# Optimization experiments

Measured on AMD Instinct MI355X. Metric: run time of the kernel, lower is better.

## Reference

```python
import jax, jax.numpy as jnp
import numpy as np

B, N, K, F, OUT = 32, 2000, 32, 64, 128

def setup_inputs() -> dict:
    key = jax.random.key(0)
    k1, k2, k3, k4, k5 = jax.random.split(key, 5)
    x = jax.random.normal(k1, (B, N, F), dtype=jnp.float32)
    neighborhood = jax.random.randint(k2, (N, K), 0, N, dtype=jnp.int64)
    distances = jax.random.uniform(k3, (N, K), dtype=jnp.float32)
    # Linear(k*(F+1), OUT): torch default init scale ~ 1/sqrt(fan_in)
    fan_in = K * (F + 1)
    W = jax.random.normal(k4, (OUT, fan_in), dtype=jnp.float32) / np.sqrt(fan_in)
    b = jax.random.normal(k5, (OUT,), dtype=jnp.float32) / np.sqrt(fan_in)
    return {"x": x, "neighborhood": neighborhood, "distances": distances, "W": W, "b": b}

def reference(x, neighborhood, distances, W, b):
    batch, seq_len, feat = x.shape          # [B, N, F]
    k = neighborhood.shape[1]
    gathered = x[:, neighborhood, :]        # [B, N, K, F] gather over sequence dim
    d = jnp.broadcast_to(distances[None, :, :, None], (batch, seq_len, k, 1))
    h = jnp.concatenate([gathered, d], axis=-1)        # [B, N, K, F+1]
    h = h.reshape(batch, seq_len, k * (feat + 1))      # [B, N, K*(F+1)]
    out = jnp.einsum('bnf,of->bno', h, W) + b          # [B, N, OUT]
    return out
```

## Files before the change

kernel.cpp:

```cpp
#include <hip/hip_runtime.h>
#include <hip/hip_bf16.h>
#include <stdint.h>

typedef __attribute__((ext_vector_type(8)))  __bf16   bf16x8;
typedef __attribute__((ext_vector_type(16))) float    f32x16;
typedef __attribute__((ext_vector_type(4)))  float    f32x4;

#define NB   32
#define NN   2000
#define NK   32
#define NF   64
#define NOUT 128
#define NSTEP 130

#define GLOBAL_AS __attribute__((address_space(1)))
#define LDS_AS    __attribute__((address_space(3)))

__global__ void kprep_x(const float* __restrict__ x, const float* __restrict__ dist,
                        __bf16* __restrict__ xb2, __bf16* __restrict__ db) {
  const int n = blockIdx.x;
  const int t = threadIdx.x;
  const int bb = t >> 3;
  const int f0 = (t & 7) << 3;
  const float* src = x + ((size_t)bb * NN + n) * NF + f0;
  f32x4 v0 = *(const f32x4*)(src);
  f32x4 v1 = *(const f32x4*)(src + 4);
  bf16x8 r;
  r[0] = (__bf16)v0[0]; r[1] = (__bf16)v0[1]; r[2] = (__bf16)v0[2]; r[3] = (__bf16)v0[3];
  r[4] = (__bf16)v1[0]; r[5] = (__bf16)v1[1]; r[6] = (__bf16)v1[2]; r[7] = (__bf16)v1[3];
  const int off = ((f0 >> 4) << 10) + (((f0 >> 3) & 1) << 9) + (bb << 4);
  *(bf16x8*)((char*)xb2 + ((size_t)n << 12) + off) = r;
  if (t < NK) db[n * NK + t] = (__bf16)dist[n * NK + t];
}

__global__ void kprep_w(const float* __restrict__ W, __bf16* __restrict__ Wf) {
  const int kstep = blockIdx.x;
  const int t = threadIdx.x;
  const int lane = t & 63;
  const int wv = t >> 6;
  const int o = wv * 32 + (lane & 31);
  const int kbase = kstep * 16 + (lane >> 5) * 8;
  bf16x8 r;
#pragma unroll
  for (int j = 0; j < 8; ++j) {
    const int kg = kbase + j;
    const int col = (kg < 2048) ? ((kg >> 6) * 65 + (kg & 63)) : ((kg - 2048) * 65 + 64);
    r[j] = (__bf16)W[(size_t)o * 2080 + col];
  }
  *(bf16x8*)(Wf + (((size_t)kstep * 256 + t) << 3)) = r;
}

__global__ __launch_bounds__(256, 4) void kmain(
    const int* __restrict__ nbrs, const float* __restrict__ bias,
    const __bf16* __restrict__ xb2, const __bf16* __restrict__ Wf,
    const __bf16* __restrict__ db, float* __restrict__ out) {
  __shared__ __align__(16) char lds[2][16384];

  const int n0   = blockIdx.x * 2;
  const int t    = threadIdx.x;
  const int lane = t & 63;
  const int w    = t >> 6;
  const int col  = lane & 31;
  const int half = lane >> 5;
  const int g    = w >> 1;
  const int c    = w & 1;

  f32x16 acc0 = {};
  f32x16 acc1 = {};

  int myidx = 0;
  if (lane < 16) myidx = nbrs[(n0 + g) * NK + lane * 2 + c];

  const __bf16* wfp = Wf + (((size_t)(w * 64 + lane)) << 3);

  auto stage = [&](int buf, int chunk) {
    const int nb = __builtin_amdgcn_readlane(myidx, chunk);
    const char* gsrc = (const char*)xb2 + ((size_t)nb << 12) + lane * 16;
    char* ldst = &lds[buf][w << 12];
#pragma unroll
    for (int q = 0; q < 4; ++q) {
      __builtin_amdgcn_global_load_lds(
          (const GLOBAL_AS uint32_t*)(gsrc + (q << 10)),
          (LDS_AS uint32_t*)(ldst + (q << 10)), 16, 0, 0);
    }
  };

  auto compute = [&](int buf, int chunk) {
#pragma unroll
    for (int cc = 0; cc < 2; ++cc) {
#pragma unroll
      for (int s = 0; s < 4; ++s) {
        const int kstep = (chunk * 2 + cc) * 4 + s;
        bf16x8 bfr = *(const bf16x8*)(wfp + ((size_t)kstep << 11));
        bf16x8 a0 = *(const bf16x8*)&lds[buf][((0 * 2 + cc) << 12) + (s << 10) + lane * 16];
        bf16x8 a1 = *(const bf16x8*)&lds[buf][((1 * 2 + cc) << 12) + (s << 10) + lane * 16];
        acc0 = __builtin_amdgcn_mfma_f32_32x32x16_bf16(a0, bfr, acc0, 0, 0, 0);
        acc1 = __builtin_amdgcn_mfma_f32_32x32x16_bf16(a1, bfr, acc1, 0, 0, 0);
      }
    }
  };

  stage(0, 0);
  int cur = 0;
  for (int chunk = 0; chunk < 15; ++chunk) {
    stage(cur ^ 1, chunk + 1);
    asm volatile("s_waitcnt vmcnt(4)" ::: "memory");
    __builtin_amdgcn_s_barrier();
    compute(cur, chunk);
    asm volatile("s_waitcnt lgkmcnt(0)" ::: "memory");
    __builtin_amdgcn_s_barrier();
    cur ^= 1;
  }
  asm volatile("s_waitcnt vmcnt(0)" ::: "memory");
  __builtin_amdgcn_s_barrier();
  compute(cur, 15);

#pragma unroll
  for (int s = 0; s < 2; ++s) {
    bf16x8 bfr = *(const bf16x8*)(wfp + ((size_t)(128 + s) << 11));
    bf16x8 dv0 = *(const bf16x8*)((const char*)db + (size_t)n0 * 64 + s * 32 + half * 16);
    bf16x8 dv1 = *(const bf16x8*)((const char*)db + ((size_t)n0 + 1) * 64 + s * 32 + half * 16);
    acc0 = __builtin_amdgcn_mfma_f32_32x32x16_bf16(dv0, bfr, acc0, 0, 0, 0);
    acc1 = __builtin_amdgcn_mfma_f32_32x32x16_bf16(dv1, bfr, acc1, 0, 0, 0);
  }

  const int o = w * 32 + col;
  const float bv = bias[o];
#pragma unroll
  for (int r = 0; r < 16; ++r) {
    const int row = (r & 3) + 8 * (r >> 2) + 4 * half;
    out[((size_t)row * NN + n0) * NOUT + o]     = acc0[r] + bv;
    out[((size_t)row * NN + n0 + 1) * NOUT + o] = acc1[r] + bv;
  }
}

extern "C" void kernel_launch(void* const* d_in, const int* in_sizes, int n_in,
                              void* d_out, int out_size, void* d_ws, size_t ws_size,
                              hipStream_t stream) {
  const float* x    = (const float*)d_in[0];
  const int*   nbrs = (const int*)d_in[1];
  const float* dist = (const float*)d_in[2];
  const float* W    = (const float*)d_in[3];
  const float* bias = (const float*)d_in[4];
  float* out = (float*)d_out;

  char* ws = (char*)d_ws;
  __bf16* xb2 = (__bf16*)(ws);
  __bf16* Wf  = (__bf16*)(ws + 8192000);
  __bf16* db  = (__bf16*)(ws + 8192000 + 532480);

  kprep_x<<<NN, 256, 0, stream>>>(x, dist, xb2, db);
  kprep_w<<<NSTEP, 256, 0, stream>>>(W, Wf);
  kmain<<<NN / 2, 256, 0, stream>>>(nbrs, bias, xb2, Wf, db, out);
}
```

Measured before the change: 62.81 us.

## Process four nodes per block with 4-stage LDS pipeline and fused prep kernel

The main kernel now computes four output nodes per block instead of two, so each W fragment loaded from global memory feeds four MFMAs instead of two. The gather of neighbor rows moves to a 4-buffer LDS ring with three chunks in flight, and W fragments are double-buffered in registers. The x and W preprocessing kernels are merged into one launch, and the x layout is changed to a simpler contiguous per-thread store. In exchange, the block count is halved and launch bounds drop to 2 blocks per CU, which reduces parallelism and occupancy.

```diff
diff --git a/kernel.cpp b/kernel.cpp
--- a/kernel.cpp
+++ b/kernel.cpp
@@ -4,7 +4,7 @@
 
 typedef __attribute__((ext_vector_type(8)))  __bf16   bf16x8;
 typedef __attribute__((ext_vector_type(16))) float    f32x16;
-typedef __attribute__((ext_vector_type(4)))  float    f32x4;
+typedef __attribute__((ext_vector_type(8)))  float    f32x8;
 
 #define NB   32
 #define NN   2000
@@ -16,112 +16,143 @@
 #define GLOBAL_AS __attribute__((address_space(1)))
 #define LDS_AS    __attribute__((address_space(3)))
 
-__global__ void kprep_x(const float* __restrict__ x, const float* __restrict__ dist,
-                        __bf16* __restrict__ xb2, __bf16* __restrict__ db) {
-  const int n = blockIdx.x;
+__global__ void kprep(const float* __restrict__ x, const float* __restrict__ dist,
+                      const float* __restrict__ W,
+                      __bf16* __restrict__ xb2, __bf16* __restrict__ db,
+                      __bf16* __restrict__ Wf) {
   const int t = threadIdx.x;
-  const int bb = t >> 3;
-  const int f0 = (t & 7) << 3;
-  const float* src = x + ((size_t)bb * NN + n) * NF + f0;
-  f32x4 v0 = *(const f32x4*)(src);
-  f32x4 v1 = *(const f32x4*)(src + 4);
-  bf16x8 r;
-  r[0] = (__bf16)v0[0]; r[1] = (__bf16)v0[1]; r[2] = (__bf16)v0[2]; r[3] = (__bf16)v0[3];
-  r[4] = (__bf16)v1[0]; r[5] = (__bf16)v1[1]; r[6] = (__bf16)v1[2]; r[7] = (__bf16)v1[3];
-  const int off = ((f0 >> 4) << 10) + (((f0 >> 3) & 1) << 9) + (bb << 4);
-  *(bf16x8*)((char*)xb2 + ((size_t)n << 12) + off) = r;
-  if (t < NK) db[n * NK + t] = (__bf16)dist[n * NK + t];
+  if (blockIdx.x < NN) {
+    const int n = blockIdx.x;
+    const int col = t & 31, half = (t >> 5) & 1, s = t >> 6;
+    const float* src = x + ((size_t)col * NN + n) * NF + s * 16 + half * 8;
+    f32x8 v = *(const f32x8*)src;
+    bf16x8 r;
+#pragma unroll
+    for (int j = 0; j < 8; ++j) r[j] = (__bf16)v[j];
+    *(bf16x8*)((char*)xb2 + ((size_t)n << 12) + t * 16) = r;
+    if (t < NK) db[n * NK + t] = (__bf16)dist[n * NK + t];
+  } else {
+    const int kstep = blockIdx.x - NN;
+    const int lane = t & 63;
+    const int wv = t >> 6;
+    const int o = wv * 32 + (lane & 31);
+    const int kbase = kstep * 16 + (lane >> 5) * 8;
+    bf16x8 r;
+#pragma unroll
+    for (int j = 0; j < 8; ++j) {
+      const int kg = kbase + j;
+      const int c = (kg < 2048) ? ((kg >> 6) * 65 + (kg & 63)) : ((kg - 2048) * 65 + 64);
+      r[j] = (__bf16)W[(size_t)o * 2080 + c];
+    }
+    *(bf16x8*)(Wf + (((size_t)kstep * 256 + t) << 3)) = r;
+  }
 }
 
-__global__ void kprep_w(const float* __restrict__ W, __bf16* __restrict__ Wf) {
-  const int kstep = blockIdx.x;
-  const int t = threadIdx.x;
-  const int lane = t & 63;
-  const int wv = t >> 6;
-  const int o = wv * 32 + (lane & 31);
-  const int kbase = kstep * 16 + (lane >> 5) * 8;
-  bf16x8 r;
-#pragma unroll
-  for (int j = 0; j < 8; ++j) {
-    const int kg = kbase + j;
-    const int col = (kg < 2048) ? ((kg >> 6) * 65 + (kg & 63)) : ((kg - 2048) * 65 + 64);
-    r[j] = (__bf16)W[(size_t)o * 2080 + col];
-  }
-  *(bf16x8*)(Wf + (((size_t)kstep * 256 + t) << 3)) = r;
-}
-
-__global__ __launch_bounds__(256, 4) void kmain(
+__global__ __launch_bounds__(256, 2) void kmain(
     const int* __restrict__ nbrs, const float* __restrict__ bias,
     const __bf16* __restrict__ xb2, const __bf16* __restrict__ Wf,
     const __bf16* __restrict__ db, float* __restrict__ out) {
-  __shared__ __align__(16) char lds[2][16384];
+  __shared__ __align__(16) char lds[4][4][4096];
 
-  const int n0   = blockIdx.x * 2;
+  const int n0   = blockIdx.x * 4;
   const int t    = threadIdx.x;
   const int lane = t & 63;
   const int w    = t >> 6;
   const int col  = lane & 31;
   const int half = lane >> 5;
-  const int g    = w >> 1;
-  const int c    = w & 1;
 
-  f32x16 acc0 = {};
-  f32x16 acc1 = {};
+  f32x16 acc0 = {}, acc1 = {}, acc2 = {}, acc3 = {};
 
   int myidx = 0;
-  if (lane < 16) myidx = nbrs[(n0 + g) * NK + lane * 2 + c];
+  if (lane < NK) myidx = nbrs[(n0 + w) * NK + lane];
 
   const __bf16* wfp = Wf + (((size_t)(w * 64 + lane)) << 3);
 
-  auto stage = [&](int buf, int chunk) {
-    const int nb = __builtin_amdgcn_readlane(myidx, chunk);
-    const char* gsrc = (const char*)xb2 + ((size_t)nb << 12) + lane * 16;
-    char* ldst = &lds[buf][w << 12];
+  auto stage = [&](int buf, int c) {
+    const int nb = __builtin_amdgcn_readlane(myidx, c);
+    const char* g = (const char*)xb2 + ((size_t)nb << 12) + lane * 16;
+    char* l = &lds[buf][w][0];
 #pragma unroll
-    for (int q = 0; q < 4; ++q) {
+    for (int q = 0; q < 4; ++q)
       __builtin_amdgcn_global_load_lds(
-          (const GLOBAL_AS uint32_t*)(gsrc + (q << 10)),
-          (LDS_AS uint32_t*)(ldst + (q << 10)), 16, 0, 0);
+          (const GLOBAL_AS uint32_t*)(g + (q << 10)),
+          (LDS_AS uint32_t*)(l + (q << 10)), 16, 0, 0);
+  };
+
+  auto loadB = [&](bf16x8* B, int i) {
+#pragma unroll
+    for (int s = 0; s < 4; ++s)
+      B[s] = *(const bf16x8*)(wfp + ((size_t)(i * 4 + s) << 11));
+  };
+
+  auto compute = [&](int buf, const bf16x8* B) {
+#pragma unroll
+    for (int s = 0; s < 4; ++s) {
+      const char* lb = &lds[buf][0][0] + (s << 10) + lane * 16;
+      bf16x8 a0 = *(const bf16x8*)(lb);
+      bf16x8 a1 = *(const bf16x8*)(lb + 4096);
+      bf16x8 a2 = *(const bf16x8*)(lb + 8192);
+      bf16x8 a3 = *(const bf16x8*)(lb + 12288);
+      acc0 = __builtin_amdgcn_mfma_f32_32x32x16_bf16(a0, B[s], acc0, 0, 0, 0);
+      acc1 = __builtin_amdgcn_mfma_f32_32x32x16_bf16(a1, B[s], acc1, 0, 0, 0);
+      acc2 = __builtin_amdgcn_mfma_f32_32x32x16_bf16(a2, B[s], acc2, 0, 0, 0);
+      acc3 = __builtin_amdgcn_mfma_f32_32x32x16_bf16(a3, B[s], acc3, 0, 0, 0);
     }
   };
 
-  auto compute = [&](int buf, int chunk) {
-#pragma unroll
-    for (int cc = 0; cc < 2; ++cc) {
-#pragma unroll
-      for (int s = 0; s < 4; ++s) {
-        const int kstep = (chunk * 2 + cc) * 4 + s;
-        bf16x8 bfr = *(const bf16x8*)(wfp + ((size_t)kstep << 11));
-        bf16x8 a0 = *(const bf16x8*)&lds[buf][((0 * 2 + cc) << 12) + (s << 10) + lane * 16];
-        bf16x8 a1 = *(const bf16x8*)&lds[buf][((1 * 2 + cc) << 12) + (s << 10) + lane * 16];
-        acc0 = __builtin_amdgcn_mfma_f32_32x32x16_bf16(a0, bfr, acc0, 0, 0, 0);
-        acc1 = __builtin_amdgcn_mfma_f32_32x32x16_bf16(a1, bfr, acc1, 0, 0, 0);
-      }
-    }
-  };
+  bf16x8 BA[4], BB[4];
 
-  stage(0, 0);
-  int cur = 0;
-  for (int chunk = 0; chunk < 15; ++chunk) {
-    stage(cur ^ 1, chunk + 1);
-    asm volatile("s_waitcnt vmcnt(4)" ::: "memory");
+  stage(0, 0); stage(1, 1); stage(2, 2);
+  loadB(BA, 0);
+
+  for (int i = 0; i < 28; i += 2) {
     __builtin_amdgcn_s_barrier();
-    compute(cur, chunk);
-    asm volatile("s_waitcnt lgkmcnt(0)" ::: "memory");
+    stage((i + 3) & 3, i + 3);
+    loadB(BB, i + 1);
+    asm volatile("s_waitcnt vmcnt(8)" ::: "memory");
     __builtin_amdgcn_s_barrier();
-    cur ^= 1;
+    compute(i & 3, BA);
+
+    __builtin_amdgcn_s_barrier();
+    stage((i + 4) & 3, i + 4);
+    loadB(BA, i + 2);
+    asm volatile("s_waitcnt vmcnt(8)" ::: "memory");
+    __builtin_amdgcn_s_barrier();
+    compute((i + 1) & 3, BB);
   }
+  __builtin_amdgcn_s_barrier();
+  stage(31 & 3, 31);
+  loadB(BB, 29);
+  asm volatile("s_waitcnt vmcnt(8)" ::: "memory");
+  __builtin_amdgcn_s_barrier();
+  compute(28 & 3, BA);
+  __builtin_amdgcn_s_barrier();
+  loadB(BA, 30);
+  asm volatile("s_waitcnt vmcnt(8)" ::: "memory");
+  __builtin_amdgcn_s_barrier();
+  compute(29 & 3, BB);
+  __builtin_amdgcn_s_barrier();
+  loadB(BB, 31);
+  asm volatile("s_waitcnt vmcnt(4)" ::: "memory");
+  __builtin_amdgcn_s_barrier();
+  compute(30 & 3, BA);
+  __builtin_amdgcn_s_barrier();
   asm volatile("s_waitcnt vmcnt(0)" ::: "memory");
   __builtin_amdgcn_s_barrier();
-  compute(cur, 15);
+  compute(31 & 3, BB);
 
 #pragma unroll
   for (int s = 0; s < 2; ++s) {
     bf16x8 bfr = *(const bf16x8*)(wfp + ((size_t)(128 + s) << 11));
-    bf16x8 dv0 = *(const bf16x8*)((const char*)db + (size_t)n0 * 64 + s * 32 + half * 16);
-    bf16x8 dv1 = *(const bf16x8*)((const char*)db + ((size_t)n0 + 1) * 64 + s * 32 + half * 16);
-    acc0 = __builtin_amdgcn_mfma_f32_32x32x16_bf16(dv0, bfr, acc0, 0, 0, 0);
-    acc1 = __builtin_amdgcn_mfma_f32_32x32x16_bf16(dv1, bfr, acc1, 0, 0, 0);
+    const char* dbase = (const char*)db + (size_t)n0 * 64 + s * 32 + half * 16;
+    bf16x8 d0 = *(const bf16x8*)(dbase);
+    bf16x8 d1 = *(const bf16x8*)(dbase + 64);
+    bf16x8 d2 = *(const bf16x8*)(dbase + 128);
+    bf16x8 d3 = *(const bf16x8*)(dbase + 192);
+    acc0 = __builtin_amdgcn_mfma_f32_32x32x16_bf16(d0, bfr, acc0, 0, 0, 0);
+    acc1 = __builtin_amdgcn_mfma_f32_32x32x16_bf16(d1, bfr, acc1, 0, 0, 0);
+    acc2 = __builtin_amdgcn_mfma_f32_32x32x16_bf16(d2, bfr, acc2, 0, 0, 0);
+    acc3 = __builtin_amdgcn_mfma_f32_32x32x16_bf16(d3, bfr, acc3, 0, 0, 0);
   }
 
   const int o = w * 32 + col;
@@ -129,8 +160,11 @@
 #pragma unroll
   for (int r = 0; r < 16; ++r) {
     const int row = (r & 3) + 8 * (r >> 2) + 4 * half;
-    out[((size_t)row * NN + n0) * NOUT + o]     = acc0[r] + bv;
-    out[((size_t)row * NN + n0 + 1) * NOUT + o] = acc1[r] + bv;
+    float* op = out + ((size_t)row * NN + n0) * NOUT + o;
+    op[0 * NOUT] = acc0[r] + bv;
+    op[1 * NOUT] = acc1[r] + bv;
+    op[2 * NOUT] = acc2[r] + bv;
+    op[3 * NOUT] = acc3[r] + bv;
   }
 }
 
@@ -149,7 +183,6 @@
   __bf16* Wf  = (__bf16*)(ws + 8192000);
   __bf16* db  = (__bf16*)(ws + 8192000 + 532480);
 
-  kprep_x<<<NN, 256, 0, stream>>>(x, dist, xb2, db);
-  kprep_w<<<NSTEP, 256, 0, stream>>>(W, Wf);
-  kmain<<<NN / 2, 256, 0, stream>>>(nbrs, bias, xb2, Wf, db, out);
+  kprep<<<NN + NSTEP, 256, 0, stream>>>(x, dist, W, xb2, db, Wf);
+  kmain<<<NN / 4, 256, 0, stream>>>(nbrs, bias, xb2, Wf, db, out);
 }
```

New measurement: 55.25 us. 12.0% less time.
